# Kernel optimization log

Measured on AMD Instinct MI355X. Metric: run time of the kernel, lower is better.

The kernel has to match this reference:

```python
import jax, jax.numpy as jnp
import numpy as np

L_TEACHER, L_STUDENT = 36, 28
B, H, S, D = 1, 16, 1024, 128
TEMPERATURE = 1.0

def _stride_prior_logits(student, teacher):
    # init: logits[i, j] = -|j - i*teacher/student|
    i = np.arange(student)[:, None].astype(np.float32)
    j = np.arange(teacher)[None, :].astype(np.float32)
    return jnp.asarray(-np.abs(j - i * teacher / student), dtype=jnp.float32)

def setup_inputs() -> dict:
    key = jax.random.key(0)
    k1, k2 = jax.random.split(key)
    ks = jax.random.normal(k1, (L_TEACHER, B, H, S, D), dtype=jnp.float32)
    vs = jax.random.normal(k2, (L_TEACHER, B, H, S, D), dtype=jnp.float32)
    logits = _stride_prior_logits(L_STUDENT, L_TEACHER)
    return {"ks": ks, "vs": vs, "attn_logits_k": logits, "attn_logits_v": logits}

def reference(ks, vs, attn_logits_k, attn_logits_v):
    # softmax over teacher-layer dim, then weighted sum across the 36 layers
    attn_k = jax.nn.softmax(attn_logits_k / TEMPERATURE, axis=-1)  # [28, 36]
    attn_v = jax.nn.softmax(attn_logits_v / TEMPERATURE, axis=-1)  # [28, 36]
    ks_pooled = jnp.einsum('lbhsd,ml->mbhsd', ks, attn_k)  # [28, B, H, S, D]
    vs_pooled = jnp.einsum('lbhsd,ml->mbhsd', vs, attn_v)  # [28, B, H, S, D]
    return (ks_pooled, vs_pooled)
```

## Files before the change

### kernel.cpp

```cpp
#include <hip/hip_runtime.h>
#include <cstddef>


constexpr int LT = 36;
constexpr int LS = 28;
constexpr int NELEM = 2097152;
constexpr int TILE_F = 64;
constexpr int TPT = NELEM / TILE_F;
constexpr int NTILES = 2 * TPT;
constexpr int NBLOCKS = 2048;
constexpr int W_STRIDE = 9 * LS * 4;

typedef __attribute__((ext_vector_type(4))) float f32x4;

__global__ __launch_bounds__(64) void softmax_kernel(
    const float* __restrict__ lgk, const float* __restrict__ lgv,
    float* __restrict__ ws)
{
    const int t = threadIdx.x;
    const int isv = t >> 5;
    const int m = t & 31;
    if (m >= LS) return;
    const float* row = (isv ? lgv : lgk) + m * LT;
    float mx = -3.4e38f;
    for (int l = 0; l < LT; ++l) mx = fmaxf(mx, row[l]);
    float s = 0.f;
    for (int l = 0; l < LT; ++l) s += expf(row[l] - mx);
    const float inv = 1.0f / s;
    float* o = ws + isv * W_STRIDE;
    for (int l = 0; l < LT; ++l)
        o[(l >> 2) * (LS * 4) + m * 4 + (l & 3)] = expf(row[l] - mx) * inv;
}

template<int LB, int G>
__device__ __forceinline__ void do_grp(const float* wq, const float d[4],
                                       float* acc)
{
    f32x4 w0, w1, w2, w3, w4, w5, w6;
    asm volatile(
        "s_load_dwordx4 %0, %[b], %[o0]\n\t"
        "s_load_dwordx4 %1, %[b], %[o1]\n\t"
        "s_load_dwordx4 %2, %[b], %[o2]\n\t"
        "s_load_dwordx4 %3, %[b], %[o3]\n\t"
        "s_load_dwordx4 %4, %[b], %[o4]\n\t"
        "s_load_dwordx4 %5, %[b], %[o5]\n\t"
        "s_load_dwordx4 %6, %[b], %[o6]\n\t"
        "s_waitcnt lgkmcnt(0)"
        : "=s"(w0), "=s"(w1), "=s"(w2), "=s"(w3), "=s"(w4), "=s"(w5), "=s"(w6)
        : [b] "s"(wq),
          [o0] "i"(LB * 448 + G * 112 + 0),
          [o1] "i"(LB * 448 + G * 112 + 16),
          [o2] "i"(LB * 448 + G * 112 + 32),
          [o3] "i"(LB * 448 + G * 112 + 48),
          [o4] "i"(LB * 448 + G * 112 + 64),
          [o5] "i"(LB * 448 + G * 112 + 80),
          [o6] "i"(LB * 448 + G * 112 + 96));

    const f32x4 W[7] = {w0, w1, w2, w3, w4, w5, w6};
#pragma unroll
    for (int k = 0; k < 7; ++k) {
        float a = acc[7 * G + k];
        a = fmaf(W[k].x, d[0], a);
        a = fmaf(W[k].y, d[1], a);
        a = fmaf(W[k].z, d[2], a);
        a = fmaf(W[k].w, d[3], a);
        acc[7 * G + k] = a;
    }
}

template<int LB>
__device__ __forceinline__ void do_lb(const float* wq,
                                      const float (*cur)[TILE_F],
                                      int lane, float* acc)
{
    float d[4];
#pragma unroll
    for (int j = 0; j < 4; ++j) d[j] = cur[4 * LB + j][lane];
    do_grp<LB, 0>(wq, d, acc);
    do_grp<LB, 1>(wq, d, acc);
    do_grp<LB, 2>(wq, d, acc);
    do_grp<LB, 3>(wq, d, acc);
}

__global__ __launch_bounds__(64) void pool_kernel(
    const float* __restrict__ ks,
    const float* __restrict__ vs,
    const float* __restrict__ ws,
    float* __restrict__ out)
{
    __shared__ float smA[LT][TILE_F];
    __shared__ float smB[LT][TILE_F];

    const int lane = threadIdx.x;

    const size_t lofs = (size_t)(lane >> 4) * NELEM + (size_t)((lane & 15) << 2);

    auto stage = [&](float (*buf)[TILE_F], int t) {
        const float* src = (t >= TPT) ? vs : ks;
        const size_t c0 = (size_t)(t & (TPT - 1)) * TILE_F;
#pragma unroll
        for (int i = 0; i < 9; ++i) {
            const float* g = src + (size_t)(4 * i) * NELEM + c0 + lofs;
            __builtin_amdgcn_global_load_lds(
                (const __attribute__((address_space(1))) void*)g,
                (__attribute__((address_space(3))) void*)&buf[4 * i][0],
                16, 0, 0);
        }
    };

    int t = blockIdx.x;
    stage(smA, t);
    asm volatile("s_waitcnt vmcnt(0)" ::: "memory");

    float (*cur)[TILE_F] = smA;
    float (*nxt)[TILE_F] = smB;

    for (;;) {
        const int tn = t + NBLOCKS;
        const bool more = (tn < NTILES);

        if (more) stage(nxt, tn);

        if (more) asm volatile("s_waitcnt vmcnt(37)" ::: "memory");
        else      asm volatile("s_waitcnt vmcnt(28)" ::: "memory");
        __builtin_amdgcn_sched_barrier(0);

        const bool isv = (t >= TPT);
        const float* wq = ws + (isv ? W_STRIDE : 0);
        const size_t c0 = (size_t)(t & (TPT - 1)) * TILE_F;
        float* dstb = out + (isv ? (size_t)LS * NELEM : (size_t)0);

        float acc[LS];
#pragma unroll
        for (int m = 0; m < LS; ++m) acc[m] = 0.f;

        do_lb<0>(wq, cur, lane, acc);
        do_lb<1>(wq, cur, lane, acc);
        do_lb<2>(wq, cur, lane, acc);
        do_lb<3>(wq, cur, lane, acc);
        do_lb<4>(wq, cur, lane, acc);
        do_lb<5>(wq, cur, lane, acc);
        do_lb<6>(wq, cur, lane, acc);
        do_lb<7>(wq, cur, lane, acc);
        do_lb<8>(wq, cur, lane, acc);

#pragma unroll
        for (int m = 0; m < LS; ++m)
            dstb[(size_t)m * NELEM + c0 + lane] = acc[m];

        if (!more) break;
        t = tn;
        float (*tmp)[TILE_F] = cur; cur = nxt; nxt = tmp;
    }
}

extern "C" void kernel_launch(void* const* d_in, const int* in_sizes, int n_in,
                              void* d_out, int out_size, void* d_ws, size_t ws_size,
                              hipStream_t stream)
{
    const float* ks  = (const float*)d_in[0];
    const float* vs  = (const float*)d_in[1];
    const float* lgk = (const float*)d_in[2];
    const float* lgv = (const float*)d_in[3];
    float* ws  = (float*)d_ws;
    float* out = (float*)d_out;

    hipLaunchKernelGGL(softmax_kernel, dim3(1), dim3(64), 0, stream,
                       lgk, lgv, ws);
    hipLaunchKernelGGL(pool_kernel, dim3(NBLOCKS), dim3(64), 0, stream,
                       ks, vs, ws, out);
}
```

Measured before the change: 244.5 us.

## Restructure pooling into per-chunk blocks with float4 accumulators and triple-buffered layer streaming

Replaces the persistent 64-thread tile loop with one 512-thread block per 2048-element chunk. Each thread owns four contiguous elements, and the kernel streams the 36 teacher layers through a 3-deep LDS ring using global_load_lds. Softmax weights are stored layer-major, so each layer needs seven scalar dwordx4 loads. Each thread holds 28 float4 accumulators and writes 128-bit coalesced stores, replacing scalar stores. The intent is more memory parallelism and wider stores. The cost is 112 accumulator VGPRs per thread, which may limit occupancy, plus per-layer scalar load waits.

```diff
diff --git a/kernel.cpp b/kernel.cpp
--- a/kernel.cpp
+++ b/kernel.cpp
@@ -5,11 +5,10 @@
 constexpr int LT = 36;
 constexpr int LS = 28;
 constexpr int NELEM = 2097152;
-constexpr int TILE_F = 64;
-constexpr int TPT = NELEM / TILE_F;
-constexpr int NTILES = 2 * TPT;
-constexpr int NBLOCKS = 2048;
-constexpr int W_STRIDE = 9 * LS * 4;
+constexpr int CHUNK = 2048;
+constexpr int NCHUNK = NELEM / CHUNK;
+constexpr int TPB = 512;
+constexpr int W_TSTRIDE = LS * LT;
 
 typedef __attribute__((ext_vector_type(4))) float f32x4;
 
@@ -27,14 +26,12 @@
     float s = 0.f;
     for (int l = 0; l < LT; ++l) s += expf(row[l] - mx);
     const float inv = 1.0f / s;
-    float* o = ws + isv * W_STRIDE;
-    for (int l = 0; l < LT; ++l)
-        o[(l >> 2) * (LS * 4) + m * 4 + (l & 3)] = expf(row[l] - mx) * inv;
+    float* o = ws + isv * W_TSTRIDE;
+    for (int l = 0; l < LT; ++l) o[l * LS + m] = expf(row[l] - mx) * inv;
 }
 
-template<int LB, int G>
-__device__ __forceinline__ void do_grp(const float* wq, const float d[4],
-                                       float* acc)
+__device__ __forceinline__ void layer_fma(const float* wlp, const float4 dv,
+                                          float4* acc)
 {
     f32x4 w0, w1, w2, w3, w4, w5, w6;
     asm volatile(
@@ -47,110 +44,83 @@
         "s_load_dwordx4 %6, %[b], %[o6]\n\t"
         "s_waitcnt lgkmcnt(0)"
         : "=s"(w0), "=s"(w1), "=s"(w2), "=s"(w3), "=s"(w4), "=s"(w5), "=s"(w6)
-        : [b] "s"(wq),
-          [o0] "i"(LB * 448 + G * 112 + 0),
-          [o1] "i"(LB * 448 + G * 112 + 16),
-          [o2] "i"(LB * 448 + G * 112 + 32),
-          [o3] "i"(LB * 448 + G * 112 + 48),
-          [o4] "i"(LB * 448 + G * 112 + 64),
-          [o5] "i"(LB * 448 + G * 112 + 80),
-          [o6] "i"(LB * 448 + G * 112 + 96));
+        : [b] "s"(wlp),
+          [o0] "i"(0),  [o1] "i"(16), [o2] "i"(32), [o3] "i"(48),
+          [o4] "i"(64), [o5] "i"(80), [o6] "i"(96));
 
     const f32x4 W[7] = {w0, w1, w2, w3, w4, w5, w6};
 #pragma unroll
-    for (int k = 0; k < 7; ++k) {
-        float a = acc[7 * G + k];
-        a = fmaf(W[k].x, d[0], a);
-        a = fmaf(W[k].y, d[1], a);
-        a = fmaf(W[k].z, d[2], a);
-        a = fmaf(W[k].w, d[3], a);
-        acc[7 * G + k] = a;
+    for (int q = 0; q < 7; ++q) {
+#pragma unroll
+        for (int j = 0; j < 4; ++j) {
+            const float w = W[q][j];
+            float4& a = acc[4 * q + j];
+            a.x = fmaf(w, dv.x, a.x);
+            a.y = fmaf(w, dv.y, a.y);
+            a.z = fmaf(w, dv.z, a.z);
+            a.w = fmaf(w, dv.w, a.w);
+        }
     }
 }
 
-template<int LB>
-__device__ __forceinline__ void do_lb(const float* wq,
-                                      const float (*cur)[TILE_F],
-                                      int lane, float* acc)
-{
-    float d[4];
-#pragma unroll
-    for (int j = 0; j < 4; ++j) d[j] = cur[4 * LB + j][lane];
-    do_grp<LB, 0>(wq, d, acc);
-    do_grp<LB, 1>(wq, d, acc);
-    do_grp<LB, 2>(wq, d, acc);
-    do_grp<LB, 3>(wq, d, acc);
-}
-
-__global__ __launch_bounds__(64) void pool_kernel(
+__global__ __launch_bounds__(TPB) void pool_kernel(
     const float* __restrict__ ks,
     const float* __restrict__ vs,
     const float* __restrict__ ws,
     float* __restrict__ out)
 {
-    __shared__ float smA[LT][TILE_F];
-    __shared__ float smB[LT][TILE_F];
+    __shared__ float buf[3][CHUNK];
 
-    const int lane = threadIdx.x;
+    const int tid  = threadIdx.x;
+    const int wv   = tid >> 6;
 
-    const size_t lofs = (size_t)(lane >> 4) * NELEM + (size_t)((lane & 15) << 2);
+    const int bid  = blockIdx.x;
+    const bool isv = (bid >= NCHUNK);
+    const float* src = isv ? vs : ks;
+    const float* wl0 = ws + (isv ? W_TSTRIDE : 0);
+    float* dstb = out + (isv ? (size_t)LS * NELEM : (size_t)0);
+    const size_t cbase = (size_t)(bid & (NCHUNK - 1)) * CHUNK;
+    const size_t toff  = cbase + (size_t)tid * 4;
 
-    auto stage = [&](float (*buf)[TILE_F], int t) {
-        const float* src = (t >= TPT) ? vs : ks;
-        const size_t c0 = (size_t)(t & (TPT - 1)) * TILE_F;
-#pragma unroll
-        for (int i = 0; i < 9; ++i) {
-            const float* g = src + (size_t)(4 * i) * NELEM + c0 + lofs;
-            __builtin_amdgcn_global_load_lds(
-                (const __attribute__((address_space(1))) void*)g,
-                (__attribute__((address_space(3))) void*)&buf[4 * i][0],
-                16, 0, 0);
-        }
+    auto stage = [&](int d, int l) {
+        const float* g = src + (size_t)l * NELEM + toff;
+        __builtin_amdgcn_global_load_lds(
+            (const __attribute__((address_space(1))) void*)g,
+            (__attribute__((address_space(3))) void*)&buf[d][wv * 256],
+            16, 0, 0);
     };
 
-    int t = blockIdx.x;
-    stage(smA, t);
+    stage(0, 0);
+    stage(1, 1);
+
+    float4 acc[LS];
+#pragma unroll
+    for (int m = 0; m < LS; ++m) acc[m] = make_float4(0.f, 0.f, 0.f, 0.f);
+
+    for (int l = 0; l < LT - 2; ++l) {
+        stage((l + 2) % 3, l + 2);
+        asm volatile("s_waitcnt vmcnt(2)" ::: "memory");
+        __builtin_amdgcn_sched_barrier(0);
+        const float4 dv = *reinterpret_cast<const float4*>(&buf[l % 3][tid * 4]);
+        layer_fma(wl0 + l * LS, dv, acc);
+    }
+    asm volatile("s_waitcnt vmcnt(1)" ::: "memory");
+    __builtin_amdgcn_sched_barrier(0);
+    {
+        const float4 dv = *reinterpret_cast<const float4*>(&buf[(LT - 2) % 3][tid * 4]);
+        layer_fma(wl0 + (LT - 2) * LS, dv, acc);
+    }
     asm volatile("s_waitcnt vmcnt(0)" ::: "memory");
-
-    float (*cur)[TILE_F] = smA;
-    float (*nxt)[TILE_F] = smB;
-
-    for (;;) {
-        const int tn = t + NBLOCKS;
-        const bool more = (tn < NTILES);
-
-        if (more) stage(nxt, tn);
-
-        if (more) asm volatile("s_waitcnt vmcnt(37)" ::: "memory");
-        else      asm volatile("s_waitcnt vmcnt(28)" ::: "memory");
-        __builtin_amdgcn_sched_barrier(0);
-
-        const bool isv = (t >= TPT);
-        const float* wq = ws + (isv ? W_STRIDE : 0);
-        const size_t c0 = (size_t)(t & (TPT - 1)) * TILE_F;
-        float* dstb = out + (isv ? (size_t)LS * NELEM : (size_t)0);
-
-        float acc[LS];
-#pragma unroll
-        for (int m = 0; m < LS; ++m) acc[m] = 0.f;
-
-        do_lb<0>(wq, cur, lane, acc);
-        do_lb<1>(wq, cur, lane, acc);
-        do_lb<2>(wq, cur, lane, acc);
-        do_lb<3>(wq, cur, lane, acc);
-        do_lb<4>(wq, cur, lane, acc);
-        do_lb<5>(wq, cur, lane, acc);
-        do_lb<6>(wq, cur, lane, acc);
-        do_lb<7>(wq, cur, lane, acc);
-        do_lb<8>(wq, cur, lane, acc);
+    __builtin_amdgcn_sched_barrier(0);
+    {
+        const float4 dv = *reinterpret_cast<const float4*>(&buf[(LT - 1) % 3][tid * 4]);
+        layer_fma(wl0 + (LT - 1) * LS, dv, acc);
+    }
 
 #pragma unroll
-        for (int m = 0; m < LS; ++m)
-            dstb[(size_t)m * NELEM + c0 + lane] = acc[m];
-
-        if (!more) break;
-        t = tn;
-        float (*tmp)[TILE_F] = cur; cur = nxt; nxt = tmp;
+    for (int m = 0; m < LS; ++m) {
+        float4* q = reinterpret_cast<float4*>(dstb + (size_t)m * NELEM + cbase);
+        q[tid] = acc[m];
     }
 }
 
@@ -167,6 +137,6 @@
 
     hipLaunchKernelGGL(softmax_kernel, dim3(1), dim3(64), 0, stream,
                        lgk, lgv, ws);
-    hipLaunchKernelGGL(pool_kernel, dim3(NBLOCKS), dim3(64), 0, stream,
+    hipLaunchKernelGGL(pool_kernel, dim3(2 * NCHUNK), dim3(TPB), 0, stream,
                        ks, vs, ws, out);
 }
```

Measured after the change: 232.6 us. 4.9% less time.
